# Optimization experiments

Measured on AMD Instinct MI355X. Metric: run time of the kernel, lower is better.

Reference implementation:

```python
import jax, jax.numpy as jnp
import numpy as np

N_NODES = 50000
N_EDGES = 200000
D = 384
R = 2  # num_relations


def setup_inputs() -> dict:
    key = jax.random.key(0)
    ks = jax.random.split(key, 16)
    inp = {
        "embeddings": jax.random.normal(ks[0], (N_NODES, D), dtype=jnp.float32),
        "edge_index": jax.random.randint(ks[1], (2, N_EDGES), 0, N_NODES, dtype=jnp.int64),
        "edge_type": jax.random.randint(ks[2], (N_EDGES,), 0, R, dtype=jnp.int64),
    }
    # RGCNConv params for 3 layers: per-relation weight, root weight, bias
    s = 1.0 / np.sqrt(D)
    for i, kk in zip((1, 2, 3), range(3)):
        inp[f"W{i}"] = jax.random.uniform(ks[3 + 3 * kk], (R, D, D), dtype=jnp.float32, minval=-s, maxval=s)
        inp[f"root{i}"] = jax.random.uniform(ks[4 + 3 * kk], (D, D), dtype=jnp.float32, minval=-s, maxval=s)
        inp[f"bias{i}"] = jnp.zeros((D,), dtype=jnp.float32)
    return inp


def _rgcn_conv(x, src, dst, edge_type, W, root, bias):
    # PyG RGCNConv with aggr='mean': for each relation, mean-aggregate neighbor
    # features over edges of that relation, then apply relation weight; plus
    # root transform and bias. We transform-then-aggregate (equivalent, linear).
    out = x @ root + bias
    for r in range(R):
        xr = x @ W[r]                                   # [N, D]
        mask = (edge_type == r).astype(x.dtype)         # [E]
        msg = xr[src] * mask[:, None]                   # [E, D] gather
        s = jax.ops.segment_sum(msg, dst, num_segments=N_NODES)    # [N, D]
        cnt = jax.ops.segment_sum(mask, dst, num_segments=N_NODES)  # [N]
        out = out + s / jnp.maximum(cnt, 1.0)[:, None]  # mean (0 if no edges)
    return out


def reference(embeddings, edge_index, edge_type, W1, root1, bias1, W2, root2, bias2, W3, root3, bias3):
    src, dst = edge_index[0], edge_index[1]
    x = jax.nn.relu(_rgcn_conv(embeddings, src, dst, edge_type, W1, root1, bias1))
    # dropout is identity in eval mode
    x = jax.nn.relu(_rgcn_conv(x, src, dst, edge_type, W2, root2, bias2))
    x = _rgcn_conv(x, src, dst, edge_type, W3, root3, bias3)
    return x
```

## Files before the change

kernel.cpp:

```cpp
#include <hip/hip_runtime.h>
#include <hip/hip_bf16.h>


#define D 384
#define NC 1152
#define BM 128
#define BN 128
#define BK 32

typedef __attribute__((ext_vector_type(8))) short short8;
typedef __attribute__((ext_vector_type(4))) float floatx4;
typedef unsigned int uint;
typedef unsigned short ushort;

__device__ __forceinline__ void load_lds16(const void* g, void* l) {
    __builtin_amdgcn_global_load_lds(
        (const __attribute__((address_space(1))) void*)g,
        (__attribute__((address_space(3))) void*)l, 16, 0, 0);
}

__device__ __forceinline__ ushort f2bf(float x) {
    __hip_bfloat16 h = __float2bfloat16(x);
    return *reinterpret_cast<ushort*>(&h);
}

__device__ __forceinline__ uint pack2(float a, float b) {
    return (uint)f2bf(a) | ((uint)f2bf(b) << 16);
}

__global__ __launch_bounds__(256) void gemm_bf16_mfma(
    const ushort* __restrict__ A, const ushort* __restrict__ BT,
    ushort* __restrict__ C, int M)
{
    __shared__ alignas(16) ushort As[BM * BK];
    __shared__ alignas(16) ushort Bs[BN * BK];

    const int tid = threadIdx.x;
    const int wave = tid >> 6;
    const int lane = tid & 63;
    const int bm = blockIdx.x * BM;
    const int bn = blockIdx.y * BN;
    const int wr = wave >> 1;
    const int wc = wave & 1;
    const int l15 = lane & 15;
    const int k8 = lane >> 4;

    floatx4 acc[4][4] = {};

    for (int k0 = 0; k0 < D; k0 += BK) {
        __syncthreads();
#pragma unroll
        for (int i = 0; i < 2; ++i) {
            const int region = i * 4 + wave;
            const int chunk = region * 64 + lane;
            const int row = chunk >> 2;
            const int c16 = chunk & 3;
            const int ga = min(bm + row, M - 1);
            load_lds16(A + (size_t)ga * D + k0 + c16 * 8, As + (size_t)region * 512);
            load_lds16(BT + (size_t)(bn + row) * D + k0 + c16 * 8, Bs + (size_t)region * 512);
        }
        __syncthreads();

        short8 af[4], bf[4];
#pragma unroll
        for (int mi = 0; mi < 4; ++mi) {
            const int m = wr * 64 + mi * 16 + l15;
            af[mi] = *(const short8*)(As + m * BK + k8 * 8);
        }
#pragma unroll
        for (int ni = 0; ni < 4; ++ni) {
            const int n = wc * 64 + ni * 16 + l15;
            bf[ni] = *(const short8*)(Bs + n * BK + k8 * 8);
        }
#pragma unroll
        for (int mi = 0; mi < 4; ++mi)
#pragma unroll
            for (int ni = 0; ni < 4; ++ni)
                acc[mi][ni] = __builtin_amdgcn_mfma_f32_16x16x32_bf16(
                    af[mi], bf[ni], acc[mi][ni], 0, 0, 0);
    }

#pragma unroll
    for (int mi = 0; mi < 4; ++mi) {
#pragma unroll
        for (int reg = 0; reg < 4; ++reg) {
            const int row = bm + wr * 64 + mi * 16 + k8 * 4 + reg;
            if (row < M) {
#pragma unroll
                for (int ni = 0; ni < 4; ++ni) {
                    const int col = bn + wc * 64 + ni * 16 + l15;
                    C[(size_t)row * NC + col] = f2bf(acc[mi][ni][reg]);
                }
            }
        }
    }
}


__global__ __launch_bounds__(256) void count_edges(
    const int* __restrict__ dst, const int* __restrict__ et,
    int* __restrict__ cntI, int E, int M)
{
    const int e = blockIdx.x * blockDim.x + threadIdx.x;
    if (e < E) atomicAdd(&cntI[(size_t)et[e] * M + dst[e]], 1);
}

__global__ __launch_bounds__(256) void finalize_cnt(
    const int* __restrict__ cntI, float* __restrict__ invc, int n)
{
    const int i = blockIdx.x * blockDim.x + threadIdx.x;
    if (i < n) invc[i] = 1.0f / (float)max(cntI[i], 1);
}

__global__ __launch_bounds__(1024) void scan_local(
    const int* __restrict__ hist, int* __restrict__ offs,
    int* __restrict__ bsums, int n)
{
    __shared__ int tmp[1024];
    const int tid = threadIdx.x;
    const int i = blockIdx.x * 1024 + tid;
    const int v = (i < n) ? hist[i] : 0;
    tmp[tid] = v;
    __syncthreads();
#pragma unroll
    for (int off = 1; off < 1024; off <<= 1) {
        const int add = (tid >= off) ? tmp[tid - off] : 0;
        __syncthreads();
        tmp[tid] += add;
        __syncthreads();
    }
    if (i < n) offs[i] = tmp[tid] - v;
    if (tid == 1023) bsums[blockIdx.x] = tmp[1023];
}

__global__ __launch_bounds__(1024) void scan_bsums(
    int* __restrict__ bsums, int* __restrict__ total_out, int nb)
{
    __shared__ int tmp[1024];
    const int tid = threadIdx.x;
    const int v = (tid < nb) ? bsums[tid] : 0;
    tmp[tid] = v;
    __syncthreads();
#pragma unroll
    for (int off = 1; off < 1024; off <<= 1) {
        const int add = (tid >= off) ? tmp[tid - off] : 0;
        __syncthreads();
        tmp[tid] += add;
        __syncthreads();
    }
    if (tid < nb) bsums[tid] = tmp[tid] - v;
    if (tid == 1023) *total_out = tmp[1023];
}

__global__ __launch_bounds__(1024) void scan_add(
    int* __restrict__ offs, const int* __restrict__ bsums, int n)
{
    const int i = blockIdx.x * 1024 + threadIdx.x;
    if (i < n) offs[i] += bsums[blockIdx.x];
}

__global__ __launch_bounds__(256) void fill_sorted(
    const int* __restrict__ src, const int* __restrict__ dst,
    const int* __restrict__ et, const int* __restrict__ offs,
    int* __restrict__ cursor, int* __restrict__ sorted, int E, int M)
{
    const int e = blockIdx.x * blockDim.x + threadIdx.x;
    if (e < E) {
        const int key = et[e] * M + dst[e];
        const int pos = offs[key] + atomicAdd(&cursor[key], 1);
        sorted[pos] = src[e];
    }
}

__global__ __launch_bounds__(256) void build_bt(
    const float* __restrict__ root1, const float* __restrict__ W1,
    const float* __restrict__ root2, const float* __restrict__ W2,
    const float* __restrict__ root3, const float* __restrict__ W3,
    ushort* __restrict__ BT)
{
    __shared__ float tile[32][33];
    const int l = blockIdx.z;
    const float* root = (l == 0) ? root1 : (l == 1) ? root2 : root3;
    const float* W    = (l == 0) ? W1    : (l == 1) ? W2    : W3;
    const int kt = blockIdx.x * 32;
    const int nt = blockIdx.y * 32;
    const int tx = threadIdx.x & 31;
    const int ty = threadIdx.x >> 5;
    const float* srcm;
    int noff;
    if (nt < D)          { srcm = root;      noff = 0; }
    else if (nt < 2 * D) { srcm = W;         noff = D; }
    else                 { srcm = W + D * D; noff = 2 * D; }
    const int n = nt - noff + tx;
#pragma unroll
    for (int i = 0; i < 4; ++i) {
        const int k = kt + ty + i * 8;
        tile[ty + i * 8][tx] = srcm[(size_t)k * D + n];
    }
    __syncthreads();
    ushort* dst = BT + (size_t)l * NC * D;
#pragma unroll
    for (int i = 0; i < 4; ++i) {
        const int nn = nt + ty + i * 8;
        const int kk = kt + tx;
        dst[(size_t)nn * D + kk] = f2bf(tile[tx][ty + i * 8]);
    }
}

__global__ __launch_bounds__(256) void cast_f32_to_bf16(
    const float* __restrict__ x, ushort* __restrict__ y, int n4)
{
    const int i = blockIdx.x * blockDim.x + threadIdx.x;
    if (i < n4) {
        const float4 v = ((const float4*)x)[i];
        uint2 o;
        o.x = pack2(v.x, v.y);
        o.y = pack2(v.z, v.w);
        ((uint2*)y)[i] = o;
    }
}

__global__ __launch_bounds__(256) void aggregate_all(
    const ushort* __restrict__ TC, const int* __restrict__ sorted,
    const int* __restrict__ offs, const float* __restrict__ invc,
    const float* __restrict__ bias, ushort* __restrict__ outb,
    float* __restrict__ outf, int M, int relu)
{
    const int wave = threadIdx.x >> 6;
    const int lane = threadIdx.x & 63;
    const int d = blockIdx.x * 4 + wave;
    if (d >= M) return;

    float v[6];
    {
        const uint* rp = (const uint*)(TC + (size_t)d * NC);
#pragma unroll
        for (int p = 0; p < 3; ++p) {
            const uint b = rp[lane + 64 * p];
            const float2 bb = *(const float2*)(bias + (lane + 64 * p) * 2);
            v[2 * p]     = __uint_as_float(b << 16) + bb.x;
            v[2 * p + 1] = __uint_as_float(b & 0xffff0000u) + bb.y;
        }
    }
#pragma unroll
    for (int r = 0; r < 2; ++r) {
        const int key = r * M + d;
        const int beg = offs[key], end = offs[key + 1];
        float g[6] = {0.f, 0.f, 0.f, 0.f, 0.f, 0.f};
        for (int i = beg; i < end; ++i) {
            const int s = sorted[i];
            const uint* tp = (const uint*)(TC + (size_t)s * NC + D + r * D);
#pragma unroll
            for (int p = 0; p < 3; ++p) {
                const uint b = tp[lane + 64 * p];
                g[2 * p]     += __uint_as_float(b << 16);
                g[2 * p + 1] += __uint_as_float(b & 0xffff0000u);
            }
        }
        const float ic = invc[key];
#pragma unroll
        for (int j = 0; j < 6; ++j) v[j] += ic * g[j];
    }
    if (relu) {
#pragma unroll
        for (int j = 0; j < 6; ++j) v[j] = fmaxf(v[j], 0.f);
    }
    if (outb) {
        uint* op = (uint*)(outb + (size_t)d * D);
#pragma unroll
        for (int p = 0; p < 3; ++p) op[lane + 64 * p] = pack2(v[2 * p], v[2 * p + 1]);
    } else {
        float2* op = (float2*)(outf + (size_t)d * D);
#pragma unroll
        for (int p = 0; p < 3; ++p)
            op[lane + 64 * p] = make_float2(v[2 * p], v[2 * p + 1]);
    }
}

extern "C" void kernel_launch(void* const* d_in, const int* in_sizes, int n_in,
                              void* d_out, int out_size, void* d_ws, size_t ws_size,
                              hipStream_t stream)
{
    const float* emb   = (const float*)d_in[0];
    const int*   eidx  = (const int*)d_in[1];
    const int*   et    = (const int*)d_in[2];
    const float* W1    = (const float*)d_in[3];
    const float* root1 = (const float*)d_in[4];
    const float* bias1 = (const float*)d_in[5];
    const float* W2    = (const float*)d_in[6];
    const float* root2 = (const float*)d_in[7];
    const float* bias2 = (const float*)d_in[8];
    const float* W3    = (const float*)d_in[9];
    const float* root3 = (const float*)d_in[10];
    const float* bias3 = (const float*)d_in[11];

    float* out = (float*)d_out;
    const int M = in_sizes[0] / D;
    const int E = in_sizes[1] / 2;
    const int* src  = eidx;
    const int* dstv = eidx + E;

    const int n = 2 * M;
    const int nb = (n + 1023) / 1024;

    char* w = (char*)d_ws;
    ushort* TC = (ushort*)w;          w += (size_t)M * NC * 2;
    ushort* Xb = (ushort*)w;          w += (size_t)M * D * 2;
    ushort* BT = (ushort*)w;          w += (size_t)3 * NC * D * 2;
    float* invcnt = (float*)w;        w += (size_t)n * 4;
    int* cntI = (int*)w;              w += (size_t)n * 4;
    int* offs = (int*)w;              w += ((size_t)n + 1) * 4;
    int* sorted = (int*)w;            w += (size_t)E * 4;
    int* bsums = (int*)w;

    hipMemsetAsync(cntI, 0, (size_t)n * sizeof(int), stream);
    count_edges<<<(E + 255) / 256, 256, 0, stream>>>(dstv, et, cntI, E, M);
    finalize_cnt<<<(n + 255) / 256, 256, 0, stream>>>(cntI, invcnt, n);
    scan_local<<<nb, 1024, 0, stream>>>(cntI, offs, bsums, n);
    scan_bsums<<<1, 1024, 0, stream>>>(bsums, offs + n, nb);
    scan_add<<<nb, 1024, 0, stream>>>(offs, bsums, n);
    hipMemsetAsync(cntI, 0, (size_t)n * sizeof(int), stream);
    fill_sorted<<<(E + 255) / 256, 256, 0, stream>>>(src, dstv, et, offs, cntI, sorted, E, M);

    build_bt<<<dim3(D / 32, NC / 32, 3), 256, 0, stream>>>(root1, W1, root2, W2, root3, W3, BT);
    cast_f32_to_bf16<<<(M * D / 4 + 255) / 256, 256, 0, stream>>>(emb, Xb, M * D / 4);

    const dim3 gg((M + BM - 1) / BM, NC / BN);
    const float* biases[3] = {bias1, bias2, bias3};
    for (int l = 0; l < 3; ++l) {
        gemm_bf16_mfma<<<gg, 256, 0, stream>>>(Xb, BT + (size_t)l * NC * D, TC, M);
        const bool last = (l == 2);
        aggregate_all<<<(M + 3) / 4, 256, 0, stream>>>(
            TC, sorted, offs, invcnt, biases[l],
            last ? nullptr : Xb, last ? out : nullptr, M, last ? 0 : 1);
    }
}
```

Measured before the change: 549.5 us.

## Double GEMM K-tile, swizzle LDS layout, and remap blocks for XCD locality

Raises the GEMM K tile from 32 to 64 so each barrier pair covers twice the MFMA work. It XOR-swizzles the 16-byte chunks in LDS to avoid bank conflicts on the fragment reads. It also replaces the 2D grid with a 1D grid that places consecutive M tiles and all N tiles of a row on the same XCD, so A rows get reuse in that XCD's L2. In exchange, LDS use doubles, and rounding the tile count up adds some early-exit blocks.

```diff
diff --git a/kernel.cpp b/kernel.cpp
--- a/kernel.cpp
+++ b/kernel.cpp
@@ -6,7 +6,8 @@
 #define NC 1152
 #define BM 128
 #define BN 128
-#define BK 32
+#define BK 64
+#define NTILES 9
 
 typedef __attribute__((ext_vector_type(8))) short short8;
 typedef __attribute__((ext_vector_type(4))) float floatx4;
@@ -35,11 +36,19 @@
     __shared__ alignas(16) ushort As[BM * BK];
     __shared__ alignas(16) ushort Bs[BN * BK];
 
+    const int b = blockIdx.x;
+    const int xcd = b & 7;
+    const int t = b >> 3;
+    const int bnt = t % NTILES;
+    const int bmt = (t / NTILES) * 8 + xcd;
+    const int Mtiles = (M + BM - 1) / BM;
+    if (bmt >= Mtiles) return;
+    const int bm = bmt * BM;
+    const int bn = bnt * BN;
+
     const int tid = threadIdx.x;
     const int wave = tid >> 6;
     const int lane = tid & 63;
-    const int bm = blockIdx.x * BM;
-    const int bn = blockIdx.y * BN;
     const int wr = wave >> 1;
     const int wc = wave & 1;
     const int l15 = lane & 15;
@@ -50,34 +59,38 @@
     for (int k0 = 0; k0 < D; k0 += BK) {
         __syncthreads();
 #pragma unroll
-        for (int i = 0; i < 2; ++i) {
-            const int region = i * 4 + wave;
-            const int chunk = region * 64 + lane;
-            const int row = chunk >> 2;
-            const int c16 = chunk & 3;
+        for (int j = 0; j < 4; ++j) {
+            const int chunk = j * 256 + wave * 64 + lane;
+            const int row = chunk >> 3;
+            const int cs = chunk & 7;
+            const int gc = cs ^ (row & 7);
             const int ga = min(bm + row, M - 1);
-            load_lds16(A + (size_t)ga * D + k0 + c16 * 8, As + (size_t)region * 512);
-            load_lds16(BT + (size_t)(bn + row) * D + k0 + c16 * 8, Bs + (size_t)region * 512);
-        }
-        __syncthreads();
-
-        short8 af[4], bf[4];
-#pragma unroll
-        for (int mi = 0; mi < 4; ++mi) {
-            const int m = wr * 64 + mi * 16 + l15;
-            af[mi] = *(const short8*)(As + m * BK + k8 * 8);
-        }
-#pragma unroll
-        for (int ni = 0; ni < 4; ++ni) {
-            const int n = wc * 64 + ni * 16 + l15;
-            bf[ni] = *(const short8*)(Bs + n * BK + k8 * 8);
-        }
-#pragma unroll
-        for (int mi = 0; mi < 4; ++mi)
-#pragma unroll
-            for (int ni = 0; ni < 4; ++ni)
-                acc[mi][ni] = __builtin_amdgcn_mfma_f32_16x16x32_bf16(
-                    af[mi], bf[ni], acc[mi][ni], 0, 0, 0);
+            load_lds16(A + (size_t)ga * D + k0 + gc * 8, As + (size_t)chunk * 8);
+            load_lds16(BT + (size_t)(bn + row) * D + k0 + gc * 8, Bs + (size_t)chunk * 8);
+        }
+        __syncthreads();
+
+#pragma unroll
+        for (int p = 0; p < 2; ++p) {
+            short8 af[4], bfr[4];
+            const int kc = p * 4 + k8;
+#pragma unroll
+            for (int mi = 0; mi < 4; ++mi) {
+                const int m = wr * 64 + mi * 16 + l15;
+                af[mi] = *(const short8*)(As + m * BK + (kc ^ (m & 7)) * 8);
+            }
+#pragma unroll
+            for (int ni = 0; ni < 4; ++ni) {
+                const int n = wc * 64 + ni * 16 + l15;
+                bfr[ni] = *(const short8*)(Bs + n * BK + (kc ^ (n & 7)) * 8);
+            }
+#pragma unroll
+            for (int mi = 0; mi < 4; ++mi)
+#pragma unroll
+                for (int ni = 0; ni < 4; ++ni)
+                    acc[mi][ni] = __builtin_amdgcn_mfma_f32_16x16x32_bf16(
+                        af[mi], bfr[ni], acc[mi][ni], 0, 0, 0);
+        }
     }
 
 #pragma unroll
@@ -325,10 +338,11 @@
     build_bt<<<dim3(D / 32, NC / 32, 3), 256, 0, stream>>>(root1, W1, root2, W2, root3, W3, BT);
     cast_f32_to_bf16<<<(M * D / 4 + 255) / 256, 256, 0, stream>>>(emb, Xb, M * D / 4);
 
-    const dim3 gg((M + BM - 1) / BM, NC / BN);
+    const int Mtiles = (M + BM - 1) / BM;
+    const int gemm_blocks = 8 * NTILES * ((Mtiles + 7) / 8);
     const float* biases[3] = {bias1, bias2, bias3};
     for (int l = 0; l < 3; ++l) {
-        gemm_bf16_mfma<<<gg, 256, 0, stream>>>(Xb, BT + (size_t)l * NC * D, TC, M);
+        gemm_bf16_mfma<<<gemm_blocks, 256, 0, stream>>>(Xb, BT + (size_t)l * NC * D, TC, M);
         const bool last = (l == 2);
         aggregate_all<<<(M + 3) / 4, 256, 0, stream>>>(
             TC, sorted, offs, invcnt, biases[l],
```

Result: faster. 498.7 us (-9.3%).
